# Kernel optimization log

Hardware: AMD Instinct MI355X
Metric: run time of the kernel (lower is better)

Reference implementation:

```python
import jax, jax.numpy as jnp
import numpy as np

N = 50000      # nodes
E = 1_600_000  # edges (avg degree 32)
D = 128        # in/hidden channels
OUT = 64       # out channels


def setup_inputs() -> dict:
    key = jax.random.key(0)
    ks = jax.random.split(key, 12)
    s = 0.08  # ~glorot scale for 128-dim
    return {
        "x": jax.random.normal(ks[0], (N, D), jnp.float32),
        "edge_index": jax.random.randint(ks[1], (2, E), 0, N, dtype=jnp.int64),
        # GCN layer 1
        "W1": jax.random.normal(ks[2], (D, D), jnp.float32) * s,
        "b1": jnp.zeros((D,), jnp.float32),
        # GraphSAGE layer 2 (mean aggregation): lin_l on neighbors, lin_r on root
        "Wl": jax.random.normal(ks[3], (D, D), jnp.float32) * s,
        "Wr": jax.random.normal(ks[4], (D, D), jnp.float32) * s,
        "bs": jnp.zeros((D,), jnp.float32),
        # GAT layer 3 (heads=1, concat=False)
        "Wg": jax.random.normal(ks[5], (D, D), jnp.float32) * s,
        "a_s": jax.random.normal(ks[6], (D,), jnp.float32) * s,
        "a_d": jax.random.normal(ks[7], (D,), jnp.float32) * s,
        "bg": jnp.zeros((D,), jnp.float32),
        # GCN output layer
        "Wo": jax.random.normal(ks[8], (D, OUT), jnp.float32) * s,
        "bo": jnp.zeros((OUT,), jnp.float32),
    }


def _self_loops(src, dst, n):
    loop = jnp.arange(n, dtype=src.dtype)
    return jnp.concatenate([src, loop]), jnp.concatenate([dst, loop])


def gcn_conv(x, W, b, src, dst, n):
    # PyG GCNConv: add self-loops, symmetric normalization D^-1/2 (A+I) D^-1/2
    s2, d2 = _self_loops(src, dst, n)
    deg = jax.ops.segment_sum(jnp.ones_like(d2, dtype=x.dtype), d2, num_segments=n)
    dinv = jnp.where(deg > 0, jax.lax.rsqrt(deg), 0.0)
    h = x @ W                         # [n, out]
    norm = dinv[s2] * dinv[d2]        # [E+n]
    out = jax.ops.segment_sum(h[s2] * norm[:, None], d2, num_segments=n)
    return out + b


def sage_conv(x, Wl, Wr, b, src, dst, n):
    # PyG SAGEConv, aggr='mean': W_l * mean_neigh + W_r * x (no self-loops)
    deg = jax.ops.segment_sum(jnp.ones_like(dst, dtype=x.dtype), dst, num_segments=n)
    agg = jax.ops.segment_sum(x[src], dst, num_segments=n)
    mean = agg / jnp.maximum(deg, 1.0)[:, None]
    return mean @ Wl + x @ Wr + b


def gat_conv(x, W, a_s, a_d, b, src, dst, n):
    # PyG GATConv heads=1, concat=False: self-loops, edge softmax over incoming edges
    h = x @ W                               # [n, out]
    s2, d2 = _self_loops(src, dst, n)
    alpha_src = h @ a_s                     # [n]
    alpha_dst = h @ a_d                     # [n]
    e = jax.nn.leaky_relu(alpha_src[s2] + alpha_dst[d2], negative_slope=0.2)
    m = jax.ops.segment_max(e, d2, num_segments=n)   # every node has a self-loop
    ex = jnp.exp(e - m[d2])
    denom = jax.ops.segment_sum(ex, d2, num_segments=n)
    alpha = ex / denom[d2]
    out = jax.ops.segment_sum(alpha[:, None] * h[s2], d2, num_segments=n)
    return out + b


def reference(x, edge_index, W1, b1, Wl, Wr, bs, Wg, a_s, a_d, bg, Wo, bo):
    src, dst = edge_index[0], edge_index[1]
    n = x.shape[0]
    # eval mode: F.dropout(training=False) is identity
    h = jax.nn.relu(gcn_conv(x, W1, b1, src, dst, n))
    h = jax.nn.relu(sage_conv(h, Wl, Wr, bs, src, dst, n))
    h = jax.nn.relu(gat_conv(h, Wg, a_s, a_d, bg, src, dst, n))
    return gcn_conv(h, Wo, bo, src, dst, n)
```

## Files before the change

### kernel.cpp

```cpp
#include <hip/hip_runtime.h>
#include <math.h>


#define BUCKET_BITS 8
#define BUCKET_SZ   256
#define NBMAX       256
#define CAP         10240

typedef short short8 __attribute__((ext_vector_type(8)));
typedef float f32x4 __attribute__((ext_vector_type(4)));

__device__ __forceinline__ float leaky02(float x) { return x > 0.0f ? x : 0.2f * x; }
__device__ __forceinline__ float bflo(unsigned u) { return __uint_as_float(u << 16); }
__device__ __forceinline__ float bfhi(unsigned u) { return __uint_as_float(u & 0xFFFF0000u); }
__device__ __forceinline__ unsigned short f2bf(float f) {
    unsigned u = __float_as_uint(f);
    u += 0x7FFFu + ((u >> 16) & 1u);
    return (unsigned short)(u >> 16);
}

template<int NO, bool AFP32, bool SCALE, bool BIASRELU, bool DUAL, bool DOTS>
__global__ __launch_bounds__(256) void mgemm_k(
    const void* __restrict__ Av, const float* __restrict__ W,
    const void* __restrict__ A1v, const float* __restrict__ W1,
    unsigned short* __restrict__ C16,
    const float* __restrict__ scale, const float* __restrict__ bias,
    const float* __restrict__ a_s, const float* __restrict__ a_d,
    float* __restrict__ as_, float* __restrict__ ad_, int n)
{
    constexpr int CT = NO / 16;
    __shared__ unsigned short Wp[128 * NO];
    const int tid = threadIdx.x;
    const int wave = tid >> 6, lane = tid & 63;
    const int q = lane >> 4, ml = lane & 15;
    const int row0 = blockIdx.x * 64 + wave * 16;
    int arow = row0 + ml; if (arow >= n) arow = n - 1;

    f32x4 acc[CT];
#pragma unroll
    for (int c = 0; c < CT; c++) acc[c] = {0.f, 0.f, 0.f, 0.f};

    for (int half = 0; half < (DUAL ? 2 : 1); half++) {
        const float* Wsrc = half ? W1 : W;
        const void* Asrc = half ? A1v : Av;
        __syncthreads();
        for (int f = tid; f < 64 * (NO / 4); f += 256) {
            const int kp = f / (NO / 4);
            const int n4 = f % (NO / 4);
            const float4 a = *(const float4*)(Wsrc + (size_t)(2 * kp) * NO + n4 * 4);
            const float4 b = *(const float4*)(Wsrc + (size_t)(2 * kp + 1) * NO + n4 * 4);
            const int k = 2 * kp, kb = k >> 5, qq = (k >> 3) & 3, p = (k & 7) >> 1;
            const float av[4] = {a.x, a.y, a.z, a.w};
            const float bv[4] = {b.x, b.y, b.z, b.w};
#pragma unroll
            for (int j = 0; j < 4; j++) {
                int col = n4 * 4 + j;
                int c = col >> 4, nl = col & 15;
                unsigned pk = (unsigned)f2bf(av[j]) | ((unsigned)f2bf(bv[j]) << 16);
                ((unsigned*)Wp)[(((kb * CT + c) * 64) + qq * 16 + nl) * 4 + p] = pk;
            }
        }
        __syncthreads();
#pragma unroll
        for (int kb = 0; kb < 4; kb++) {
            short8 afr;
            if (AFP32) {
                const float* Af = (const float*)Asrc + (size_t)arow * 128 + kb * 32 + q * 8;
#pragma unroll
                for (int j = 0; j < 8; j++) afr[j] = (short)f2bf(Af[j]);
            } else {
                afr = *(const short8*)((const unsigned short*)Asrc +
                                       (size_t)arow * 128 + kb * 32 + q * 8);
            }
#pragma unroll
            for (int c = 0; c < CT; c++) {
                short8 bfr = *(const short8*)(Wp + ((size_t)(kb * CT + c) * 64 + lane) * 8);
                acc[c] = __builtin_amdgcn_mfma_f32_16x16x32_bf16(afr, bfr, acc[c], 0, 0, 0);
            }
        }
    }

    if (DOTS) {
        float ps[4] = {0.f, 0.f, 0.f, 0.f}, pd[4] = {0.f, 0.f, 0.f, 0.f};
#pragma unroll
        for (int c = 0; c < CT; c++) {
            float sv = a_s[c * 16 + ml], dv = a_d[c * 16 + ml];
#pragma unroll
            for (int r = 0; r < 4; r++) {
                ps[r] = fmaf(acc[c][r], sv, ps[r]);
                pd[r] = fmaf(acc[c][r], dv, pd[r]);
            }
        }
#pragma unroll
        for (int off = 1; off < 16; off <<= 1) {
#pragma unroll
            for (int r = 0; r < 4; r++) {
                ps[r] += __shfl_xor(ps[r], off, 64);
                pd[r] += __shfl_xor(pd[r], off, 64);
            }
        }
        if (ml == 0) {
#pragma unroll
            for (int r = 0; r < 4; r++) {
                int row = row0 + q * 4 + r;
                if (row < n) { as_[row] = ps[r]; ad_[row] = pd[r]; }
            }
        }
    }

    float sc[4];
    if (SCALE) {
#pragma unroll
        for (int r = 0; r < 4; r++) {
            int row = row0 + q * 4 + r;
            sc[r] = scale[row < n ? row : 0];
        }
    }
#pragma unroll
    for (int c = 0; c < CT; c++) {
        float bv = BIASRELU ? bias[c * 16 + ml] : 0.0f;
#pragma unroll
        for (int r = 0; r < 4; r++) {
            int row = row0 + q * 4 + r;
            if (row < n) {
                float v = acc[c][r];
                if (SCALE) v *= sc[r];
                if (BIASRELU) v = fmaxf(v + bv, 0.0f);
                C16[(size_t)row * NO + c * 16 + ml] = f2bf(v);
            }
        }
    }
}

__global__ void binit_k(int* __restrict__ bcur, int nb) {
    int t = threadIdx.x;
    if (t < nb) bcur[t] = t * CAP;
}

#define PART_CH 4096
__global__ __launch_bounds__(256) void part_k(
    const int* __restrict__ src, const int* __restrict__ dst,
    int* __restrict__ bcur, unsigned long long* __restrict__ part, int nE)
{
    __shared__ int cnt[NBMAX];
    __shared__ int cur[NBMAX];
    const int base = blockIdx.x * PART_CH;
    const int t = threadIdx.x;
    cnt[t] = 0;
    __syncthreads();
    int d[PART_CH / 256], s[PART_CH / 256];
#pragma unroll
    for (int j = 0; j < PART_CH / 256; j++) {
        int e = base + j * 256 + t;
        if (e < nE) {
            d[j] = dst[e]; s[j] = src[e];
            atomicAdd(&cnt[d[j] >> BUCKET_BITS], 1);
        } else d[j] = -1;
    }
    __syncthreads();
    {
        int c = cnt[t];
        cur[t] = c ? atomicAdd(&bcur[t], c) : 0;
    }
    __syncthreads();
#pragma unroll
    for (int j = 0; j < PART_CH / 256; j++) {
        if (d[j] >= 0) {
            int p = atomicAdd(&cur[d[j] >> BUCKET_BITS], 1);
            part[p] = ((unsigned long long)(unsigned)d[j] << 32) | (unsigned)s[j];
        }
    }
}

__global__ __launch_bounds__(256) void bscan_k(const int* __restrict__ bcur,
                                               int* __restrict__ bofs, int nb) {
    __shared__ int sm[256];
    const int t = threadIdx.x;
    int v = (t < nb) ? (bcur[t] - t * CAP) : 0;
    sm[t] = v;
    __syncthreads();
    for (int off = 1; off < 256; off <<= 1) {
        int tv = (t >= off) ? sm[t - off] : 0;
        __syncthreads();
        sm[t] += tv;
        __syncthreads();
    }
    if (t < nb) {
        bofs[t] = sm[t] - v;
        if (t == nb - 1) bofs[nb] = sm[t];
    }
}

__global__ __launch_bounds__(256) void csr_k(
    const unsigned long long* __restrict__ part, const int* __restrict__ bcur,
    const int* __restrict__ bofs, int* __restrict__ rowptr, int* __restrict__ srcs,
    float* __restrict__ dinv, float* __restrict__ invm, int n, int nE)
{
    __shared__ int lcnt[BUCKET_SZ];
    __shared__ int sm[BUCKET_SZ];
    __shared__ int lcur[BUCKET_SZ];
    const int b = blockIdx.x;
    const int t = threadIdx.x;
    const int base_in = b * CAP;
    const int cntE = bcur[b] - base_in;
    const int base_out = bofs[b];

    lcnt[t] = 0;
    __syncthreads();
#pragma unroll 4
    for (int e = t; e < cntE; e += 256) {
        int dl = (int)(part[base_in + e] >> 32) & (BUCKET_SZ - 1);
        atomicAdd(&lcnt[dl], 1);
    }
    __syncthreads();
    int v = lcnt[t];
    sm[t] = v;
    __syncthreads();
    for (int off = 1; off < 256; off <<= 1) {
        int tv = (t >= off) ? sm[t - off] : 0;
        __syncthreads();
        sm[t] += tv;
        __syncthreads();
    }
    const int excl = sm[t] - v;
    const int node = (b << BUCKET_BITS) + t;
    if (node < n) {
        rowptr[node] = base_out + excl;
        float dg = (float)v;
        dinv[node] = rsqrtf(dg + 1.0f);
        invm[node] = 1.0f / fmaxf(dg, 1.0f);
        if (node == n - 1) rowptr[n] = nE;
    }
    lcur[t] = excl;
    __syncthreads();
#pragma unroll 4
    for (int e = t; e < cntE; e += 256) {
        unsigned long long w = part[base_in + e];
        int dl = (int)(w >> 32) & (BUCKET_SZ - 1);
        int pos = atomicAdd(&lcur[dl], 1);
        srcs[base_out + pos] = (int)(unsigned)w;
    }
}

template<int F, int MODE>
__global__ __launch_bounds__(256) void gatherbf_k(
    const unsigned short* __restrict__ H16, float* __restrict__ outf,
    unsigned short* __restrict__ out16,
    const int* __restrict__ rowptr, const int* __restrict__ srcs,
    const float* __restrict__ dinv, const float* __restrict__ as_,
    const float* __restrict__ ad_, const float* __restrict__ bias, int n)
{
    constexpr int LPN = F / 4;
    constexpr int NPB = 256 / LPN;
    const int node = blockIdx.x * NPB + (int)(threadIdx.x / LPN);
    const int lane = (int)(threadIdx.x & (LPN - 1));
    if (node >= n) return;
    const int beg = rowptr[node], end = rowptr[node + 1];

    const uint2* __restrict__ H2 = (const uint2*)H16;
    float4 acc = make_float4(0.f, 0.f, 0.f, 0.f);

    float ad_d = 0.f, rden = 0.f, sw = 0.f;
    if (MODE == 2) {
        ad_d = ad_[node];
        float self_e = __expf(leaky02(as_[node] + ad_d));
        float psum = 0.f;
        for (int k = beg + lane; k < end; k += LPN)
            psum += __expf(leaky02(as_[srcs[k]] + ad_d));
#pragma unroll
        for (int off = LPN / 2; off > 0; off >>= 1) psum += __shfl_xor(psum, off, 64);
        rden = 1.0f / (psum + self_e);
        sw = self_e * rden;
    }

    int k = beg;
    for (; k + 8 <= end; k += 8) {
        unsigned sidx[8]; float asv[8];
#pragma unroll
        for (int j = 0; j < 8; j++) sidx[j] = (unsigned)srcs[k + j];
        if (MODE == 2) {
#pragma unroll
            for (int j = 0; j < 8; j++) asv[j] = as_[sidx[j]];
        }
        uint2 h[8];
#pragma unroll
        for (int j = 0; j < 8; j++) h[j] = H2[(size_t)sidx[j] * LPN + lane];
#pragma unroll
        for (int j = 0; j < 8; j++) {
            if (MODE == 2) {
                float w0 = __expf(leaky02(asv[j] + ad_d)) * rden;
                acc.x = fmaf(w0, bflo(h[j].x), acc.x);
                acc.y = fmaf(w0, bfhi(h[j].x), acc.y);
                acc.z = fmaf(w0, bflo(h[j].y), acc.z);
                acc.w = fmaf(w0, bfhi(h[j].y), acc.w);
            } else {
                acc.x += bflo(h[j].x); acc.y += bfhi(h[j].x);
                acc.z += bflo(h[j].y); acc.w += bfhi(h[j].y);
            }
        }
    }
    if (k < end) {
        unsigned sidx[8]; float asv[8]; bool act[8];
#pragma unroll
        for (int j = 0; j < 8; j++) {
            int kk = k + j;
            act[j] = (kk < end);
            sidx[j] = (unsigned)srcs[act[j] ? kk : (end - 1)];
        }
        if (MODE == 2) {
#pragma unroll
            for (int j = 0; j < 8; j++) asv[j] = as_[sidx[j]];
        }
        uint2 h[8];
#pragma unroll
        for (int j = 0; j < 8; j++) h[j] = H2[(size_t)sidx[j] * LPN + lane];
#pragma unroll
        for (int j = 0; j < 8; j++) {
            float w0;
            if (MODE == 2) w0 = act[j] ? __expf(leaky02(asv[j] + ad_d)) * rden : 0.0f;
            else           w0 = act[j] ? 1.0f : 0.0f;
            acc.x = fmaf(w0, bflo(h[j].x), acc.x);
            acc.y = fmaf(w0, bfhi(h[j].x), acc.y);
            acc.z = fmaf(w0, bflo(h[j].y), acc.z);
            acc.w = fmaf(w0, bfhi(h[j].y), acc.w);
        }
    }

    const size_t oi = (size_t)node * LPN + lane;
    float4 r;
    if (MODE == 0) {
        float sc = dinv[node];
        r.x = acc.x * sc; r.y = acc.y * sc; r.z = acc.z * sc; r.w = acc.w * sc;
    } else {
        uint2 su = H2[oi];
        float s0 = bflo(su.x), s1 = bfhi(su.x), s2 = bflo(su.y), s3 = bfhi(su.y);
        float4 bv = ((const float4*)bias)[lane];
        if (MODE == 2) {
            r.x = acc.x + sw * s0 + bv.x;
            r.y = acc.y + sw * s1 + bv.y;
            r.z = acc.z + sw * s2 + bv.z;
            r.w = acc.w + sw * s3 + bv.w;
            r.x = fmaxf(r.x, 0.f); r.y = fmaxf(r.y, 0.f);
            r.z = fmaxf(r.z, 0.f); r.w = fmaxf(r.w, 0.f);
        } else {
            float dv = dinv[node];
            r.x = dv * (acc.x + s0) + bv.x;
            r.y = dv * (acc.y + s1) + bv.y;
            r.z = dv * (acc.z + s2) + bv.z;
            r.w = dv * (acc.w + s3) + bv.w;
            if (MODE == 1) {
                r.x = fmaxf(r.x, 0.f); r.y = fmaxf(r.y, 0.f);
                r.z = fmaxf(r.z, 0.f); r.w = fmaxf(r.w, 0.f);
            }
        }
    }
    if (MODE == 3) {
        ((float4*)outf)[oi] = r;
    } else {
        ushort4 qv; qv.x = f2bf(r.x); qv.y = f2bf(r.y); qv.z = f2bf(r.z); qv.w = f2bf(r.w);
        ((ushort4*)out16)[oi] = qv;
    }
}

extern "C" void kernel_launch(void* const* d_in, const int* in_sizes, int n_in,
                              void* d_out, int out_size, void* d_ws, size_t ws_size,
                              hipStream_t stream)
{
    const float* x   = (const float*)d_in[0];
    const int*   ei  = (const int*)d_in[1];
    const float* W1  = (const float*)d_in[2];
    const float* b1  = (const float*)d_in[3];
    const float* Wl  = (const float*)d_in[4];
    const float* Wr  = (const float*)d_in[5];
    const float* bs  = (const float*)d_in[6];
    const float* Wg  = (const float*)d_in[7];
    const float* a_s = (const float*)d_in[8];
    const float* a_d = (const float*)d_in[9];
    const float* bg  = (const float*)d_in[10];
    const float* Wo  = (const float*)d_in[11];
    const float* bo  = (const float*)d_in[12];

    const int n  = in_sizes[0] / 128;
    const int nE = in_sizes[1] / 2;
    const int* src = ei;
    const int* dst = ei + nE;

    char* w = (char*)d_ws;
    auto alloc = [&](size_t bytes) { char* p = w; w += (bytes + 255) & ~(size_t)255; return p; };
    unsigned short* S0 = (unsigned short*)alloc((size_t)n * 128 * 2);
    unsigned short* S1 = (unsigned short*)alloc((size_t)n * 128 * 2);
    unsigned short* S2 = (unsigned short*)alloc((size_t)n * 128 * 2);
    const int nbv = (n + BUCKET_SZ - 1) / BUCKET_SZ;
    unsigned long long* part = (unsigned long long*)alloc((size_t)nbv * CAP * 8);
    int*   srcs   = (int*)alloc((size_t)nE * 4);
    int*   rowptr = (int*)alloc((size_t)(n + 1) * 4);
    int*   bofs   = (int*)alloc((NBMAX + 1) * 4);
    int*   bcur   = (int*)alloc(NBMAX * 4);
    float* dinv   = (float*)alloc((size_t)n * 4);
    float* invm   = (float*)alloc((size_t)n * 4);
    float* as_    = (float*)alloc((size_t)n * 4);
    float* ad_    = (float*)alloc((size_t)n * 4);

    const int TB = 256;
    auto cdiv = [](long long a, long long b) { return (int)((a + b - 1) / b); };
    const int nb     = nbv;
    const int gPart  = cdiv(nE, PART_CH);
    const int gGemm  = cdiv(n, 64);
    const int gGa128 = cdiv(n, 8);
    const int gGa64  = cdiv(n, 16);

    binit_k<<<1, 256, 0, stream>>>(bcur, nb);
    part_k<<<gPart, TB, 0, stream>>>(src, dst, bcur, part, nE);
    bscan_k<<<1, 256, 0, stream>>>(bcur, bofs, nb);
    csr_k<<<nb, TB, 0, stream>>>(part, bcur, bofs, rowptr, srcs, dinv, invm, n, nE);

    mgemm_k<128, true, true, false, false, false><<<gGemm, TB, 0, stream>>>(
        x, W1, nullptr, nullptr, S0, dinv, nullptr, nullptr, nullptr, nullptr, nullptr, n);
    gatherbf_k<128, 1><<<gGa128, TB, 0, stream>>>(S0, nullptr, S1, rowptr, srcs,
                                                  dinv, nullptr, nullptr, b1, n);

    gatherbf_k<128, 0><<<gGa128, TB, 0, stream>>>(S1, nullptr, S0, rowptr, srcs,
                                                  invm, nullptr, nullptr, nullptr, n);
    mgemm_k<128, false, false, true, true, false><<<gGemm, TB, 0, stream>>>(
        S0, Wl, S1, Wr, S2, nullptr, bs, nullptr, nullptr, nullptr, nullptr, n);

    mgemm_k<128, false, false, false, false, true><<<gGemm, TB, 0, stream>>>(
        S2, Wg, nullptr, nullptr, S1, nullptr, nullptr, a_s, a_d, as_, ad_, n);
    gatherbf_k<128, 2><<<gGa128, TB, 0, stream>>>(S1, nullptr, S0, rowptr, srcs,
                                                  nullptr, as_, ad_, bg, n);

    mgemm_k<64, false, true, false, false, false><<<gGemm, TB, 0, stream>>>(
        S0, Wo, nullptr, nullptr, S2, dinv, nullptr, nullptr, nullptr, nullptr, nullptr, n);
    gatherbf_k<64, 3><<<gGa64, TB, 0, stream>>>(S2, (float*)d_out, nullptr, rowptr, srcs,
                                                dinv, nullptr, nullptr, bo, n);
}
```

Before: 385.5 us.

## Stage block edge indices and GAT weights in LDS, widen gather to 16B loads

The gather kernel now cooperatively loads each block's contiguous CSR source indices into shared memory, and for GAT it caches the per-edge exp weights computed in the softmax pass so the second pass reuses them instead of recomputing exp and re-reading as_. Each lane now handles 8 bf16 features with 16-byte loads, so twice as many nodes share a block, and normalisation by the softmax denominator is applied once at the end. This adds block-wide barriers and an overflow path for blocks whose edges exceed the LDS capacity.

New measurement: 369.8 us. -4.1%, faster.

```diff
diff --git a/kernel.cpp b/kernel.cpp
--- a/kernel.cpp
+++ b/kernel.cpp
@@ -6,9 +6,12 @@
 #define BUCKET_SZ   256
 #define NBMAX       256
 #define CAP         10240
+#define CAPE        2048
 
 typedef short short8 __attribute__((ext_vector_type(8)));
 typedef float f32x4 __attribute__((ext_vector_type(4)));
+typedef unsigned int u32x4 __attribute__((ext_vector_type(4)));
+typedef unsigned short u16x8 __attribute__((ext_vector_type(8)));
 
 __device__ __forceinline__ float leaky02(float x) { return x > 0.0f ? x : 0.2f * x; }
 __device__ __forceinline__ float bflo(unsigned u) { return __uint_as_float(u << 16); }
@@ -242,6 +245,82 @@
     }
 }
 
+template<int LPN, int MODE, bool OV>
+__device__ __forceinline__ void gath_loop(
+    const u32x4* __restrict__ H4, const int* __restrict__ srcs,
+    const int* lsrc, const float* lw, const float* __restrict__ as_,
+    float ad_d, int beg, int end, int beg_blk, int lane, float* acc)
+{
+    const u32x4* __restrict__ Hl = H4 + lane;
+    int k = beg;
+    for (; k + 8 <= end; k += 8) {
+        unsigned sidx[8]; float wv[8];
+#pragma unroll
+        for (int j = 0; j < 8; j++) {
+            int ofs = k + j - beg_blk;
+            if (OV) {
+                int ofc = ofs < CAPE ? ofs : CAPE - 1;
+                int s = (ofs < CAPE) ? lsrc[ofc] : srcs[k + j];
+                sidx[j] = (unsigned)s;
+                if (MODE == 2)
+                    wv[j] = (ofs < CAPE) ? lw[ofc] : __expf(leaky02(as_[s] + ad_d));
+            } else {
+                sidx[j] = (unsigned)lsrc[ofs];
+                if (MODE == 2) wv[j] = lw[ofs];
+            }
+        }
+        u32x4 h[8];
+#pragma unroll
+        for (int j = 0; j < 8; j++) h[j] = Hl[(size_t)sidx[j] * LPN];
+#pragma unroll
+        for (int j = 0; j < 8; j++) {
+#pragma unroll
+            for (int c = 0; c < 4; c++) {
+                if (MODE == 2) {
+                    acc[2 * c]     = fmaf(wv[j], bflo(h[j][c]), acc[2 * c]);
+                    acc[2 * c + 1] = fmaf(wv[j], bfhi(h[j][c]), acc[2 * c + 1]);
+                } else {
+                    acc[2 * c]     += bflo(h[j][c]);
+                    acc[2 * c + 1] += bfhi(h[j][c]);
+                }
+            }
+        }
+    }
+    if (k < end) {
+        unsigned sidx[8]; float wv[8];
+#pragma unroll
+        for (int j = 0; j < 8; j++) {
+            int kk = k + j;
+            bool act = kk < end;
+            int kc = act ? kk : end - 1;
+            int ofs = kc - beg_blk;
+            int s; float w0 = 1.0f;
+            if (OV) {
+                int ofc = ofs < CAPE ? ofs : CAPE - 1;
+                s = (ofs < CAPE) ? lsrc[ofc] : srcs[kc];
+                if (MODE == 2)
+                    w0 = (ofs < CAPE) ? lw[ofc] : __expf(leaky02(as_[s] + ad_d));
+            } else {
+                s = lsrc[ofs];
+                if (MODE == 2) w0 = lw[ofs];
+            }
+            sidx[j] = (unsigned)s;
+            wv[j] = act ? w0 : 0.0f;
+        }
+        u32x4 h[8];
+#pragma unroll
+        for (int j = 0; j < 8; j++) h[j] = Hl[(size_t)sidx[j] * LPN];
+#pragma unroll
+        for (int j = 0; j < 8; j++) {
+#pragma unroll
+            for (int c = 0; c < 4; c++) {
+                acc[2 * c]     = fmaf(wv[j], bflo(h[j][c]), acc[2 * c]);
+                acc[2 * c + 1] = fmaf(wv[j], bfhi(h[j][c]), acc[2 * c + 1]);
+            }
+        }
+    }
+}
+
 template<int F, int MODE>
 __global__ __launch_bounds__(256) void gatherbf_k(
     const unsigned short* __restrict__ H16, float* __restrict__ outf,
@@ -250,115 +329,100 @@
     const float* __restrict__ dinv, const float* __restrict__ as_,
     const float* __restrict__ ad_, const float* __restrict__ bias, int n)
 {
-    constexpr int LPN = F / 4;
+    constexpr int LPN = F / 8;
     constexpr int NPB = 256 / LPN;
-    const int node = blockIdx.x * NPB + (int)(threadIdx.x / LPN);
-    const int lane = (int)(threadIdx.x & (LPN - 1));
-    if (node >= n) return;
-    const int beg = rowptr[node], end = rowptr[node + 1];
-
-    const uint2* __restrict__ H2 = (const uint2*)H16;
-    float4 acc = make_float4(0.f, 0.f, 0.f, 0.f);
+    __shared__ int lsrc[CAPE];
+    __shared__ float lw[(MODE == 2) ? CAPE : 1];
+
+    const int tid = (int)threadIdx.x;
+    const int node0 = (int)blockIdx.x * NPB;
+    const int nodeN = min(node0 + NPB, n);
+    const int beg_blk = rowptr[node0];
+    const int end_blk = rowptr[nodeN];
+    const int cnt = end_blk - beg_blk;
+    const int cl = min(cnt, CAPE);
+    for (int i = tid; i < cl; i += 256) lsrc[i] = srcs[beg_blk + i];
+    __syncthreads();
+
+    const int node = node0 + tid / LPN;
+    const int lane = tid & (LPN - 1);
+    const bool alive = node < n;
+    int beg = 0, end = 0;
+    if (alive) { beg = rowptr[node]; end = rowptr[node + 1]; }
 
     float ad_d = 0.f, rden = 0.f, sw = 0.f;
     if (MODE == 2) {
-        ad_d = ad_[node];
-        float self_e = __expf(leaky02(as_[node] + ad_d));
-        float psum = 0.f;
-        for (int k = beg + lane; k < end; k += LPN)
-            psum += __expf(leaky02(as_[srcs[k]] + ad_d));
-#pragma unroll
-        for (int off = LPN / 2; off > 0; off >>= 1) psum += __shfl_xor(psum, off, 64);
-        rden = 1.0f / (psum + self_e);
-        sw = self_e * rden;
-    }
-
-    int k = beg;
-    for (; k + 8 <= end; k += 8) {
-        unsigned sidx[8]; float asv[8];
-#pragma unroll
-        for (int j = 0; j < 8; j++) sidx[j] = (unsigned)srcs[k + j];
-        if (MODE == 2) {
-#pragma unroll
-            for (int j = 0; j < 8; j++) asv[j] = as_[sidx[j]];
-        }
-        uint2 h[8];
-#pragma unroll
-        for (int j = 0; j < 8; j++) h[j] = H2[(size_t)sidx[j] * LPN + lane];
-#pragma unroll
-        for (int j = 0; j < 8; j++) {
-            if (MODE == 2) {
-                float w0 = __expf(leaky02(asv[j] + ad_d)) * rden;
-                acc.x = fmaf(w0, bflo(h[j].x), acc.x);
-                acc.y = fmaf(w0, bfhi(h[j].x), acc.y);
-                acc.z = fmaf(w0, bflo(h[j].y), acc.z);
-                acc.w = fmaf(w0, bfhi(h[j].y), acc.w);
-            } else {
-                acc.x += bflo(h[j].x); acc.y += bfhi(h[j].x);
-                acc.z += bflo(h[j].y); acc.w += bfhi(h[j].y);
-            }
-        }
-    }
-    if (k < end) {
-        unsigned sidx[8]; float asv[8]; bool act[8];
-#pragma unroll
-        for (int j = 0; j < 8; j++) {
-            int kk = k + j;
-            act[j] = (kk < end);
-            sidx[j] = (unsigned)srcs[act[j] ? kk : (end - 1)];
-        }
-        if (MODE == 2) {
-#pragma unroll
-            for (int j = 0; j < 8; j++) asv[j] = as_[sidx[j]];
-        }
-        uint2 h[8];
-#pragma unroll
-        for (int j = 0; j < 8; j++) h[j] = H2[(size_t)sidx[j] * LPN + lane];
-#pragma unroll
-        for (int j = 0; j < 8; j++) {
-            float w0;
-            if (MODE == 2) w0 = act[j] ? __expf(leaky02(asv[j] + ad_d)) * rden : 0.0f;
-            else           w0 = act[j] ? 1.0f : 0.0f;
-            acc.x = fmaf(w0, bflo(h[j].x), acc.x);
-            acc.y = fmaf(w0, bfhi(h[j].x), acc.y);
-            acc.z = fmaf(w0, bflo(h[j].y), acc.z);
-            acc.w = fmaf(w0, bfhi(h[j].y), acc.w);
-        }
-    }
-
-    const size_t oi = (size_t)node * LPN + lane;
-    float4 r;
+        if (alive) {
+            ad_d = ad_[node];
+            float self_e = __expf(leaky02(as_[node] + ad_d));
+            float psum = 0.f;
+            for (int kk = beg + lane; kk < end; kk += LPN) {
+                int ofs = kk - beg_blk;
+                int s = (ofs < CAPE) ? lsrc[ofs < CAPE ? ofs : 0] : srcs[kk];
+                float wv = __expf(leaky02(as_[s] + ad_d));
+                if (ofs < CAPE) lw[ofs] = wv;
+                psum += wv;
+            }
+#pragma unroll
+            for (int off = LPN / 2; off > 0; off >>= 1)
+                psum += __shfl_xor(psum, off, 64);
+            rden = 1.0f / (psum + self_e);
+            sw = self_e * rden;
+        }
+        __syncthreads();
+    }
+
+    float acc[8];
+#pragma unroll
+    for (int j = 0; j < 8; j++) acc[j] = 0.f;
+
+    const u32x4* __restrict__ H4 = (const u32x4*)H16;
+    if (alive) {
+        if (cnt <= CAPE)
+            gath_loop<LPN, MODE, false>(H4, srcs, lsrc, lw, as_, ad_d,
+                                        beg, end, beg_blk, lane, acc);
+        else
+            gath_loop<LPN, MODE, true>(H4, srcs, lsrc, lw, as_, ad_d,
+                                       beg, end, beg_blk, lane, acc);
+    }
+    if (!alive) return;
+
+    const size_t orow = (size_t)node * LPN + lane;
+    float r[8];
     if (MODE == 0) {
         float sc = dinv[node];
-        r.x = acc.x * sc; r.y = acc.y * sc; r.z = acc.z * sc; r.w = acc.w * sc;
+#pragma unroll
+        for (int j = 0; j < 8; j++) r[j] = acc[j] * sc;
     } else {
-        uint2 su = H2[oi];
-        float s0 = bflo(su.x), s1 = bfhi(su.x), s2 = bflo(su.y), s3 = bfhi(su.y);
-        float4 bv = ((const float4*)bias)[lane];
+        u32x4 su = H4[orow];
+        float sv[8];
+#pragma unroll
+        for (int c = 0; c < 4; c++) { sv[2 * c] = bflo(su[c]); sv[2 * c + 1] = bfhi(su[c]); }
+        const float4* b4 = (const float4*)bias;
+        float4 ba = b4[lane * 2], bb = b4[lane * 2 + 1];
+        float bv[8] = {ba.x, ba.y, ba.z, ba.w, bb.x, bb.y, bb.z, bb.w};
         if (MODE == 2) {
-            r.x = acc.x + sw * s0 + bv.x;
-            r.y = acc.y + sw * s1 + bv.y;
-            r.z = acc.z + sw * s2 + bv.z;
-            r.w = acc.w + sw * s3 + bv.w;
-            r.x = fmaxf(r.x, 0.f); r.y = fmaxf(r.y, 0.f);
-            r.z = fmaxf(r.z, 0.f); r.w = fmaxf(r.w, 0.f);
+#pragma unroll
+            for (int j = 0; j < 8; j++)
+                r[j] = fmaxf(fmaf(rden, acc[j], fmaf(sw, sv[j], bv[j])), 0.f);
         } else {
             float dv = dinv[node];
-            r.x = dv * (acc.x + s0) + bv.x;
-            r.y = dv * (acc.y + s1) + bv.y;
-            r.z = dv * (acc.z + s2) + bv.z;
-            r.w = dv * (acc.w + s3) + bv.w;
-            if (MODE == 1) {
-                r.x = fmaxf(r.x, 0.f); r.y = fmaxf(r.y, 0.f);
-                r.z = fmaxf(r.z, 0.f); r.w = fmaxf(r.w, 0.f);
+#pragma unroll
+            for (int j = 0; j < 8; j++) {
+                r[j] = dv * (acc[j] + sv[j]) + bv[j];
+                if (MODE == 1) r[j] = fmaxf(r[j], 0.f);
             }
         }
     }
     if (MODE == 3) {
-        ((float4*)outf)[oi] = r;
+        float4 ra = {r[0], r[1], r[2], r[3]}, rb = {r[4], r[5], r[6], r[7]};
+        ((float4*)outf)[orow * 2]     = ra;
+        ((float4*)outf)[orow * 2 + 1] = rb;
     } else {
-        ushort4 qv; qv.x = f2bf(r.x); qv.y = f2bf(r.y); qv.z = f2bf(r.z); qv.w = f2bf(r.w);
-        ((ushort4*)out16)[oi] = qv;
+        u16x8 qv;
+#pragma unroll
+        for (int j = 0; j < 8; j++) qv[j] = f2bf(r[j]);
+        ((u16x8*)out16)[orow] = qv;
     }
 }
 
@@ -406,8 +470,8 @@
     const int nb     = nbv;
     const int gPart  = cdiv(nE, PART_CH);
     const int gGemm  = cdiv(n, 64);
-    const int gGa128 = cdiv(n, 8);
-    const int gGa64  = cdiv(n, 16);
+    const int gGa128 = cdiv(n, 16);
+    const int gGa64  = cdiv(n, 32);
 
     binit_k<<<1, 256, 0, stream>>>(bcur, nb);
     part_k<<<gPart, TB, 0, stream>>>(src, dst, bcur, part, nE);
```
